# Kernel optimization log

Measured on AMD Instinct MI355X. Metric: run time of the kernel, lower is better.

## Reference

```python
import jax, jax.numpy as jnp
import numpy as np

DG = 8            # deformable_groups
MAX_RES = 10.0    # max_residual_magnitude
K = 9             # 3x3 kernel positions


def conv3(x, w, b):
    y = jax.lax.conv_general_dilated(x, w, (1, 1), [(1, 1), (1, 1)],
                                     dimension_numbers=('NCHW', 'OIHW', 'NCHW'))
    return y + b[None, :, None, None]


def lrelu(v):
    return jnp.where(v >= 0, v, 0.1 * v)


def deform_conv2d(x, offset, mask, weight, bias):
    # x: [B,C,H,W]; offset: [B,2*DG*K,H,W] (per group, K points, (y,x) interleaved)
    # mask: [B,DG*K,H,W]; weight: [O,C,3,3]; stride=1, pad=1, dil=1, groups=1
    B, C, H, W = x.shape
    Cg = C // DG
    off = offset.reshape(B, DG, K, 2, H, W)
    dtype = x.dtype
    dy = (jnp.arange(K) // 3 - 1).astype(dtype)
    dx = (jnp.arange(K) % 3 - 1).astype(dtype)
    py = off[:, :, :, 0] + jnp.arange(H, dtype=dtype)[None, None, None, :, None] + dy[None, None, :, None, None]
    px = off[:, :, :, 1] + jnp.arange(W, dtype=dtype)[None, None, None, None, :] + dx[None, None, :, None, None]
    y0 = jnp.floor(py)
    x0 = jnp.floor(px)
    x_flat = x.reshape(B, DG, Cg, H * W)
    m = mask.reshape(B, DG, K, H, W)
    acc = jnp.zeros((B, DG, Cg, K, H, W), dtype=dtype)
    for iy, wy in ((y0, y0 + 1.0 - py), (y0 + 1.0, py - y0)):
        for ix, wx in ((x0, x0 + 1.0 - px), (x0 + 1.0, px - x0)):
            valid = (iy >= 0) & (iy < H) & (ix >= 0) & (ix < W)
            yi = jnp.clip(iy, 0, H - 1).astype(jnp.int32)
            xi = jnp.clip(ix, 0, W - 1).astype(jnp.int32)
            idx = (yi * W + xi).reshape(B, DG, 1, K * H * W)
            g = jnp.take_along_axis(x_flat, idx, axis=3).reshape(B, DG, Cg, K, H, W)
            wgt = (wy * wx * valid.astype(dtype) * m)[:, :, None]  # mask folded in
            acc = acc + g * wgt
    O = weight.shape[0]
    out = jnp.einsum('bgckhw,ogck->bohw', acc, weight.reshape(O, DG, Cg, K))
    return out + bias[None, :, None, None]


def setup_inputs() -> dict:
    key = jax.random.key(0)
    ks = jax.random.split(key, 12)
    B, C, H, W = 4, 64, 128, 128
    inp = {
        'x': jax.random.normal(ks[0], (B, C, H, W), jnp.float32),
        'x_warped0': jax.random.normal(ks[1], (B, C, H, W), jnp.float32),
        'x_current': jax.random.normal(ks[2], (B, C, H, W), jnp.float32),
        'flow0': jax.random.normal(ks[3], (B, 2, H, W), jnp.float32),
        'w1': jax.random.normal(ks[4], (64, 130, 3, 3), jnp.float32) * 0.05,
        'b1': jnp.zeros((64,), jnp.float32),
        'w2': jax.random.normal(ks[5], (64, 64, 3, 3), jnp.float32) * 0.05,
        'b2': jnp.zeros((64,), jnp.float32),
        'w3': jax.random.normal(ks[6], (64, 64, 3, 3), jnp.float32) * 0.05,
        'b3': jnp.zeros((64,), jnp.float32),
        'w4': jax.random.normal(ks[7], (216, 64, 3, 3), jnp.float32) * 0.05,
        'b4': jnp.zeros((216,), jnp.float32),
        'weight': jax.random.normal(ks[8], (64, 64, 3, 3), jnp.float32) * 0.05,
        'bias': jnp.zeros((64,), jnp.float32),
    }
    return inp


def reference(x, x_warped0, x_current, flow0, w1, b1, w2, b2, w3, b3, w4, b4, weight, bias):
    # conv_offset stack on cat([x_warped0, x_current, flow0])
    feat = jnp.concatenate([x_warped0, x_current, flow0], axis=1)  # [B, 2C+2, H, W]
    o = lrelu(conv3(feat, w1, b1))
    o = lrelu(conv3(o, w2, b2))
    o = lrelu(conv3(o, w3, b3))
    o = conv3(o, w4, b4)  # [B, 3*K*DG, H, W]
    out1, out2, mask = jnp.split(o, 3, axis=1)
    offset = MAX_RES * jnp.tanh(jnp.concatenate([out1, out2], axis=1))  # [B, 2*K*DG, H, W]
    # flows[0].flip(1).repeat(1, K*DG, 1, 1): (y,x) flow tiled over all sample points
    offset = offset + jnp.tile(flow0[:, ::-1], (1, K * DG, 1, 1))
    mask = jax.nn.sigmoid(mask)
    return deform_conv2d(x, offset, mask, weight, bias)
```

## Files before the change

### kernel.cpp

```cpp
#include <hip/hip_runtime.h>
#include <math.h>

#define HH 128
#define WW 128
#define BB 4
#define HW (HH*WW)

typedef unsigned short u16;
typedef unsigned int u32;
typedef __bf16 bf16x8 __attribute__((ext_vector_type(8)));
typedef float f32x4 __attribute__((ext_vector_type(4)));

__device__ __forceinline__ u16 f2bf(float x) {
    u32 u = __float_as_uint(x);
    return (u16)((u + 0x7fffu + ((u >> 16) & 1u)) >> 16);
}
__device__ __forceinline__ float bf2f(u16 h) {
    return __uint_as_float(((u32)h) << 16);
}
__device__ __forceinline__ bf16x8 ld8(const u16* p) {
    union { uint4 u; bf16x8 v; } c;
    c.u = *(const uint4*)p;
    return c.v;
}
__device__ __forceinline__ bf16x8 cvt8(uint4 u) {
    union { uint4 u; bf16x8 v; } c;
    c.u = u;
    return c.v;
}

__global__ void split_w_k(const float* __restrict__ src, u16* __restrict__ dh,
                          u16* __restrict__ dl, int OC, int OCpad, int CIN, int CINpad)
{
    const int i = blockIdx.x * 256 + threadIdx.x;
    const int tot = OCpad * 9 * CINpad;
    if (i >= tot) return;
    const int oc = i / (9 * CINpad);
    const int r = i - oc * 9 * CINpad;
    const int tap = r / CINpad;
    const int cin = r - tap * CINpad;
    float v = 0.f;
    if (oc < OC && cin < CIN) v = src[((size_t)oc * CIN + cin) * 9 + tap];
    const u16 h = f2bf(v);
    dh[i] = h;
    dl[i] = f2bf(v - bf2f(h));
}

__global__ void pad_bias_k(const float* __restrict__ b, float* __restrict__ bp)
{
    const int i = blockIdx.x * 256 + threadIdx.x;
    if (i < 256) bp[i] = (i < 216) ? b[i] : 0.f;
}

__global__ void pack_dw_k(const float* __restrict__ wt, u16* __restrict__ Apack)
{
    const int i = blockIdx.x * 256 + threadIdx.x;
    if (i >= 36864) return;
    const int jj = i & 7;
    const int fr = (i >> 3) & 15;
    const int m  = (i >> 7) & 3;
    const int fq = (i >> 9) & 3;
    const int kk = i >> 11;
    const int oc = m * 16 + fr;
    const int j  = kk * 32 + fq * 8 + jj;
    const int tap = j >> 3, c = j & 7;
    const int g = tap / 9, kt = tap - g * 9;
    const int ch = g * 8 + c;
    Apack[i] = f2bf(wt[((size_t)oc * 64 + ch) * 9 + kt]);
}

template<int CREC>
__global__ __launch_bounds__(256) void pack_x_k(
    const float* __restrict__ A, const float* __restrict__ B2,
    const float* __restrict__ C3, u16* __restrict__ dst)
{
    const int i = blockIdx.x * 256 + threadIdx.x;
    const int b = i >> 14;
    const int px = i & 16383;
    u16* rec = dst + (size_t)i * (CREC * 2);

#pragma unroll
    for (int g = 0; g < CREC / 32; ++g) {
#pragma unroll
        for (int cb = 0; cb < 4; ++cb) {
            u32 hwv[4], lwv[4];
#pragma unroll
            for (int p = 0; p < 4; ++p) {
                float v[2];
#pragma unroll
                for (int e = 0; e < 2; ++e) {
                    const int c = g * 32 + cb * 8 + p * 2 + e;
                    float vv;
                    if (c < 64)       vv = A[((size_t)(b * 64 + c)) * HW + px];
                    else if (c < 128) vv = B2[((size_t)(b * 64 + c - 64)) * HW + px];
                    else if (c < 130) vv = C3[((size_t)(b * 2 + c - 128)) * HW + px];
                    else              vv = 0.f;
                    v[e] = vv;
                }
                const u16 h0 = f2bf(v[0]), h1 = f2bf(v[1]);
                const u16 l0 = f2bf(v[0] - bf2f(h0)), l1 = f2bf(v[1] - bf2f(h1));
                hwv[p] = (u32)h0 | ((u32)h1 << 16);
                lwv[p] = (u32)l0 | ((u32)l1 << 16);
            }
            uint4 H; H.x = hwv[0]; H.y = hwv[1]; H.z = hwv[2]; H.w = hwv[3];
            uint4 L; L.x = lwv[0]; L.y = lwv[1]; L.z = lwv[2]; L.w = lwv[3];
            *(uint4*)(rec + g * 64 + cb * 16)     = H;
            *(uint4*)(rec + g * 64 + cb * 16 + 8) = L;
        }
    }
}

template<int NCHUNK, int KGLAST, int MODE, bool RELU, bool PACKOUT, int MINW>
__global__ __launch_bounds__(256, MINW) void conv_pk_k(
    const u16* __restrict__ Xp, const u16* __restrict__ Wh, const u16* __restrict__ Wl,
    const float* __restrict__ bias, float* __restrict__ outf, u16* __restrict__ outp,
    int OCreal)
{
    const int ROWS = (MODE == 1) ? 8 : 4;
    const int NPX = (ROWS + 2) * 18;
    __shared__ u16 Xs[NPX * 136];
    const int CINpad = (NCHUNK - 1) * 64 + KGLAST * 32;
    const int CRECU16 = CINpad * 2;

    const int tile = blockIdx.x;
    const int h0 = (tile >> 3) * ROWS;
    const int w0 = (tile & 7) * 16;
    const int b = blockIdx.z;
    const int t = threadIdx.x;
    const int lane = t & 63, wv = t >> 6;
    const int fr = lane & 15, fq = lane >> 4;

    const int mg = wv >> 1, rg = wv & 1;
    const int mbase = (MODE == 1) ? (blockIdx.y * 8 + mg * 4) : 0;

    f32x4 acc0[4];
    f32x4 acc1[4][4];
    if (MODE == 0) {
        const float4 bv = *(const float4*)(bias + wv * 16 + 4 * fq);
#pragma unroll
        for (int n = 0; n < 4; ++n) {
            acc0[n][0] = bv.x; acc0[n][1] = bv.y; acc0[n][2] = bv.z; acc0[n][3] = bv.w;
        }
    } else {
#pragma unroll
        for (int m = 0; m < 4; ++m) {
            const float4 bv = *(const float4*)(bias + (mbase + m) * 16 + 4 * fq);
#pragma unroll
            for (int n = 0; n < 4; ++n) {
                acc1[m][n][0] = bv.x; acc1[m][n][1] = bv.y;
                acc1[m][n][2] = bv.z; acc1[m][n][3] = bv.w;
            }
        }
    }

    const u16* WhL = Wh + (size_t)fr * 9 * CINpad + 8 * fq;
    const u16* WlL = Wl + (size_t)fr * 9 * CINpad + 8 * fq;

#pragma unroll
    for (int chunk = 0; chunk < NCHUNK; ++chunk) {
        const int nkg = (chunk == NCHUNK - 1) ? KGLAST : 2;
        const int nu = nkg * 8;
        __syncthreads();
        for (int s = t; s < NPX * nu; s += 256) {
            const int px = s / nu, o = s - px * nu;
            const int hy = px / 18, hx = px - hy * 18;
            const int gy = h0 + hy - 1, gx = w0 + hx - 1;
            uint4 v; v.x = 0; v.y = 0; v.z = 0; v.w = 0;
            if (gy >= 0 && gy < HH && gx >= 0 && gx < WW)
                v = *(const uint4*)(Xp + ((size_t)(b * HW + gy * WW + gx)) * CRECU16
                                       + chunk * 128 + o * 8);
            *(uint4*)(Xs + px * 136 + o * 8) = v;
        }
        __syncthreads();

        if (MODE == 0) {
#pragma unroll
            for (int tap = 0; tap < 9; ++tap) {
                const int ky = tap / 3, kx = tap % 3;
#pragma unroll
                for (int kg = 0; kg < 2; ++kg) {
                    if (kg >= nkg) break;
                    const size_t off = (size_t)(wv * 144 + tap) * CINpad + chunk * 64 + kg * 32;
                    const bf16x8 Ah = ld8(WhL + off);
                    const bf16x8 Al = ld8(WlL + off);
#pragma unroll
                    for (int n = 0; n < 4; ++n) {
                        const int hp = (n + ky) * 18 + fr + kx;
                        const u16* Bp = Xs + hp * 136 + kg * 64 + fq * 16;
                        const bf16x8 Bh = ld8(Bp);
                        const bf16x8 Bl = ld8(Bp + 8);
                        acc0[n] = __builtin_amdgcn_mfma_f32_16x16x32_bf16(Ah, Bh, acc0[n], 0, 0, 0);
                        acc0[n] = __builtin_amdgcn_mfma_f32_16x16x32_bf16(Ah, Bl, acc0[n], 0, 0, 0);
                        acc0[n] = __builtin_amdgcn_mfma_f32_16x16x32_bf16(Al, Bh, acc0[n], 0, 0, 0);
                    }
                }
            }
        } else {
            auto PF = [&](int tap, bf16x8 (&Dh)[8], bf16x8 (&Dl)[8]) {
#pragma unroll
                for (int kg = 0; kg < 2; ++kg)
#pragma unroll
                    for (int m = 0; m < 4; ++m) {
                        const size_t off = (size_t)((mbase + m) * 144 + tap) * CINpad
                                         + chunk * 64 + kg * 32;
                        Dh[kg * 4 + m] = ld8(WhL + off);
                        Dl[kg * 4 + m] = ld8(WlL + off);
                    }
            };
            auto CMP = [&](int tap, bf16x8 (&Dh)[8], bf16x8 (&Dl)[8]) {
                const int ky = tap / 3, kx = tap - 3 * ky;
#pragma unroll
                for (int kg = 0; kg < 2; ++kg) {
#pragma unroll
                    for (int n = 0; n < 4; ++n) {
                        const int hp = (rg * 4 + n + ky) * 18 + fr + kx;
                        const u16* Bp = Xs + hp * 136 + kg * 64 + fq * 16;
                        const bf16x8 Bh = ld8(Bp);
                        const bf16x8 Bl = ld8(Bp + 8);
#pragma unroll
                        for (int m = 0; m < 4; ++m) {
                            acc1[m][n] = __builtin_amdgcn_mfma_f32_16x16x32_bf16(Dh[kg * 4 + m], Bh, acc1[m][n], 0, 0, 0);
                            acc1[m][n] = __builtin_amdgcn_mfma_f32_16x16x32_bf16(Dh[kg * 4 + m], Bl, acc1[m][n], 0, 0, 0);
                            acc1[m][n] = __builtin_amdgcn_mfma_f32_16x16x32_bf16(Dl[kg * 4 + m], Bh, acc1[m][n], 0, 0, 0);
                        }
                    }
                }
            };

            bf16x8 PaH[8], PaL[8], PbH[8], PbL[8];
            PF(0, PaH, PaL);
#pragma unroll 1
            for (int tp = 0; tp < 4; ++tp) {
                PF(2 * tp + 1, PbH, PbL);
                CMP(2 * tp, PaH, PaL);
                PF(2 * tp + 2, PaH, PaL);
                CMP(2 * tp + 1, PbH, PbL);
            }
            CMP(8, PaH, PaL);
        }
    }

    if (MODE == 1) {
#pragma unroll
        for (int m = 0; m < 4; ++m)
#pragma unroll
            for (int n = 0; n < 4; ++n)
#pragma unroll
                for (int i = 0; i < 4; ++i) {
                    const int oc = (mbase + m) * 16 + 4 * fq + i;
                    if (oc < OCreal) {
                        float v = acc1[m][n][i];
                        if (RELU) v = (v >= 0.f) ? v : 0.1f * v;
                        outf[((size_t)(b * OCreal + oc)) * HW + (h0 + rg * 4 + n) * WW + w0 + fr] = v;
                    }
                }
    } else if (!PACKOUT) {
#pragma unroll
        for (int n = 0; n < 4; ++n)
#pragma unroll
            for (int i = 0; i < 4; ++i) {
                const int oc = wv * 16 + 4 * fq + i;
                if (oc < OCreal) {
                    float v = acc0[n][i];
                    if (RELU) v = (v >= 0.f) ? v : 0.1f * v;
                    outf[((size_t)(b * OCreal + oc)) * HW + (h0 + n) * WW + w0 + fr] = v;
                }
            }
    } else {
        __syncthreads();
        const int coff = (wv >> 1) * 64 + (((wv << 1) + (fq >> 1)) & 3) * 16 + ((fq & 1) << 2);
#pragma unroll
        for (int n = 0; n < 4; ++n) {
            u16 hh[4], ll[4];
#pragma unroll
            for (int i = 0; i < 4; ++i) {
                float v = acc0[n][i];
                if (RELU) v = (v >= 0.f) ? v : 0.1f * v;
                hh[i] = f2bf(v);
                ll[i] = f2bf(v - bf2f(hh[i]));
            }
            uint2 H, L;
            H.x = (u32)hh[0] | ((u32)hh[1] << 16);
            H.y = (u32)hh[2] | ((u32)hh[3] << 16);
            L.x = (u32)ll[0] | ((u32)ll[1] << 16);
            L.y = (u32)ll[2] | ((u32)ll[3] << 16);
            const int pxe = n * 16 + fr;
            u16* E = Xs + pxe * 136 + coff;
            *(uint2*)E = H;
            *(uint2*)(E + 8) = L;
        }
        __syncthreads();
        for (int i = t; i < 1024; i += 256) {
            const int px = i >> 4, o = i & 15;
            const uint4 v = *(const uint4*)(Xs + px * 136 + o * 8);
            const int gp = (h0 + (px >> 4)) * WW + w0 + (px & 15);
            *(uint4*)(outp + ((size_t)(b * HW + gp)) * 128 + o * 8) = v;
        }
    }
}

__global__ __launch_bounds__(256) void pack_xb_k(
    const float* __restrict__ x, uint4* __restrict__ xqb)
{
    const int i = blockIdx.x * 256 + threadIdx.x;
    const int pix = i & (HW - 1);
    const int g = (i >> 14) & 7;
    const int b = i >> 17;
    const float* xp = x + ((size_t)(b * 64 + g * 8)) * HW + pix;
    u32 w[4];
#pragma unroll
    for (int c2 = 0; c2 < 4; ++c2) {
        const u16 l = f2bf(xp[(size_t)(2 * c2) * HW]);
        const u16 h = f2bf(xp[(size_t)(2 * c2 + 1) * HW]);
        w[c2] = (u32)l | ((u32)h << 16);
    }
    uint4 v; v.x = w[0]; v.y = w[1]; v.z = w[2]; v.w = w[3];
    xqb[(size_t)(b * 8 + g) * HW + pix] = v;
}

__device__ __forceinline__ unsigned pk_bf16(float lo, float hi) {
    unsigned a = __float_as_uint(lo), b = __float_as_uint(hi);
    return ((a + 0x8000u) >> 16) | ((b + 0x8000u) & 0xffff0000u);
}

__global__ __launch_bounds__(256, 4) void deform_fused_k(
    const uint4* __restrict__ xqb, const float* __restrict__ o4,
    const float* __restrict__ flow, const uint4* __restrict__ Apack,
    const float* __restrict__ bias, float* __restrict__ out)
{
    __shared__ u16 sv[32 * 584];

    const int bid = blockIdx.x;
    const int b = bid >> 9;
    const int pix0 = (bid & 511) << 5;
    const int t = threadIdx.x;

    {
        const int gpx = t & 31, g = t >> 5;
        const int pix = pix0 + gpx;
        const int h = pix >> 7, w = pix & (WW - 1);
        const float fy = flow[((size_t)b * 2 + 1) * HW + pix];
        const float fx = flow[((size_t)b * 2 + 0) * HW + pix];
        const float* ob = o4 + (size_t)b * 216 * HW + pix;
        const uint4* qg = xqb + (size_t)(b * 8 + g) * HW;

        int   code[9];
        float w00[9], w01[9], w10[9], w11[9];

#pragma unroll
        for (int k = 0; k < 9; ++k) {
            const float oy = ob[(size_t)(g * 18 + k * 2) * HW];
            const float ox = ob[(size_t)(g * 18 + k * 2 + 1) * HW];
            float mm = ob[(size_t)(144 + g * 9 + k) * HW];
            mm = __builtin_amdgcn_rcpf(1.f + __expf(-mm));

            const float ay = fabsf(oy), ax = fabsf(ox);
            const float ey = __expf(-2.f * ay), ex = __expf(-2.f * ax);
            float ty = (1.f - ey) * __builtin_amdgcn_rcpf(1.f + ey);
            float tx = (1.f - ex) * __builtin_amdgcn_rcpf(1.f + ex);
            ty = copysignf(ty, oy); tx = copysignf(tx, ox);

            const float ppy = 10.f * ty + fy + (float)(h + k / 3 - 1);
            const float ppx = 10.f * tx + fx + (float)(w + k % 3 - 1);

            const float y0f = floorf(ppy), x0f = floorf(ppx);
            const float ly = ppy - y0f, lx = ppx - x0f;
            const int iy0 = (int)y0f, ix0 = (int)x0f;
            const int iy1 = iy0 + 1,  ix1 = ix0 + 1;

            const float vy0 = (iy0 >= 0 && iy0 < HH) ? 1.f : 0.f;
            const float vy1 = (iy1 >= 0 && iy1 < HH) ? 1.f : 0.f;
            const float vx0 = (ix0 >= 0 && ix0 < WW) ? 1.f : 0.f;
            const float vx1 = (ix1 >= 0 && ix1 < WW) ? 1.f : 0.f;

            const int cy0 = min(max(iy0, 0), HH - 1);
            const int cy1 = min(max(iy1, 0), HH - 1);
            const int cx0 = min(max(ix0, 0), WW - 1);
            const int cx1 = min(max(ix1, 0), WW - 1);

            w00[k] = (1.f - ly) * (1.f - lx) * vy0 * vx0 * mm;
            w01[k] = (1.f - ly) * lx         * vy0 * vx1 * mm;
            w10[k] = ly         * (1.f - lx) * vy1 * vx0 * mm;
            w11[k] = ly         * lx         * vy1 * vx1 * mm;

            code[k] = (cy0 * WW + cx0) | ((cx1 - cx0) << 14) | ((cy1 - cy0) << 15);
        }

        u16* svp = sv + gpx * 584 + g * 72;
#pragma unroll
        for (int k = 0; k < 9; ++k) {
            const int i00 = code[k] & 16383;
            const int i01 = i00 + ((code[k] >> 14) & 1);
            const int i10 = i00 + (((code[k] >> 15) & 1) << 7);
            const int i11 = i10 + ((code[k] >> 14) & 1);

            const uint4 A4 = qg[i00];
            const uint4 B4 = qg[i01];
            const uint4 C4 = qg[i10];
            const uint4 D4 = qg[i11];
            const float W00 = w00[k], W01 = w01[k], W10 = w10[k], W11 = w11[k];

            uint4 P;
            u32 pw[4];
#pragma unroll
            for (int c2 = 0; c2 < 4; ++c2) {
                const u32 aw = (&A4.x)[c2], bw = (&B4.x)[c2];
                const u32 cw = (&C4.x)[c2], dw = (&D4.x)[c2];
                const float alo = __uint_as_float(aw << 16), ahi = __uint_as_float(aw & 0xffff0000u);
                const float blo = __uint_as_float(bw << 16), bhi = __uint_as_float(bw & 0xffff0000u);
                const float clo = __uint_as_float(cw << 16), chi = __uint_as_float(cw & 0xffff0000u);
                const float dlo = __uint_as_float(dw << 16), dhi = __uint_as_float(dw & 0xffff0000u);
                const float slo = W00 * alo + W01 * blo + W10 * clo + W11 * dlo;
                const float shi = W00 * ahi + W01 * bhi + W10 * chi + W11 * dhi;
                pw[c2] = pk_bf16(slo, shi);
            }
            P.x = pw[0]; P.y = pw[1]; P.z = pw[2]; P.w = pw[3];
            *(uint4*)(svp + (size_t)k * 8) = P;
        }
    }
    __syncthreads();

    {
        const int lane = t & 63, wv = t >> 6;
        const int fr = lane & 15, fq = lane >> 4;

        f32x4 acc[2];
#pragma unroll
        for (int n = 0; n < 2; ++n) { acc[n][0] = 0.f; acc[n][1] = 0.f; acc[n][2] = 0.f; acc[n][3] = 0.f; }

#pragma unroll
        for (int kk = 0; kk < 18; ++kk) {
            const bf16x8 A = cvt8(Apack[((kk * 4 + fq) * 4 + wv) * 16 + fr]);
#pragma unroll
            for (int n = 0; n < 2; ++n) {
                const bf16x8 Bf = ld8(sv + (size_t)(n * 16 + fr) * 584 + kk * 32 + fq * 8);
                acc[n] = __builtin_amdgcn_mfma_f32_16x16x32_bf16(A, Bf, acc[n], 0, 0, 0);
            }
        }

        const float4 bv = *(const float4*)(bias + wv * 16 + 4 * fq);
        const float bb[4] = { bv.x, bv.y, bv.z, bv.w };
#pragma unroll
        for (int n = 0; n < 2; ++n) {
            const int pix = pix0 + n * 16 + fr;
#pragma unroll
            for (int i = 0; i < 4; ++i) {
                const int oc = wv * 16 + 4 * fq + i;
                out[((size_t)b * 64 + oc) * HW + pix] = acc[n][i] + bb[i];
            }
        }
    }
}

extern "C" void kernel_launch(void* const* d_in, const int* in_sizes, int n_in,
                              void* d_out, int out_size, void* d_ws, size_t ws_size,
                              hipStream_t stream)
{
    const float* x     = (const float*)d_in[0];
    const float* xw    = (const float*)d_in[1];
    const float* xc    = (const float*)d_in[2];
    const float* flow  = (const float*)d_in[3];
    const float* w1    = (const float*)d_in[4];
    const float* b1    = (const float*)d_in[5];
    const float* w2    = (const float*)d_in[6];
    const float* b2    = (const float*)d_in[7];
    const float* w3    = (const float*)d_in[8];
    const float* b3    = (const float*)d_in[9];
    const float* w4    = (const float*)d_in[10];
    const float* b4    = (const float*)d_in[11];
    const float* wt    = (const float*)d_in[12];
    const float* bias  = (const float*)d_in[13];
    float* out = (float*)d_out;

    char* ws = (char*)d_ws;
    u16*   X1p  = (u16*)(ws);
    float* o4   = (float*)(ws);
    u16*   buf1 = (u16*)(ws + 56623104);
    u16*   buf2 = (u16*)(ws + 73400320);
    u16* Apack = (u16*)(ws + 90177536);
    u16* W1h = (u16*)(ws + 90251264);
    u16* W1l = (u16*)(ws + 90435584);
    u16* W2h = (u16*)(ws + 90619904);
    u16* W2l = (u16*)(ws + 90693632);
    u16* W3h = (u16*)(ws + 90767360);
    u16* W3l = (u16*)(ws + 90841088);
    u16* W4h = (u16*)(ws + 90914816);
    u16* W4l = (u16*)(ws + 91209728);
    float* b4p = (float*)(ws + 91504640);

    const dim3 blk(256);

    split_w_k<<<dim3((64 * 9 * 160 + 255) / 256), blk, 0, stream>>>(w1, W1h, W1l, 64, 64, 130, 160);
    split_w_k<<<dim3((64 * 9 * 64 + 255) / 256), blk, 0, stream>>>(w2, W2h, W2l, 64, 64, 64, 64);
    split_w_k<<<dim3((64 * 9 * 64 + 255) / 256), blk, 0, stream>>>(w3, W3h, W3l, 64, 64, 64, 64);
    split_w_k<<<dim3((256 * 9 * 64 + 255) / 256), blk, 0, stream>>>(w4, W4h, W4l, 216, 256, 64, 64);
    pad_bias_k<<<dim3(1), blk, 0, stream>>>(b4, b4p);
    pack_dw_k<<<dim3(144), blk, 0, stream>>>(wt, Apack);

    pack_x_k<160><<<dim3(BB * HW / 256), blk, 0, stream>>>(xw, xc, flow, X1p);
    conv_pk_k<3, 1, 0, true, true, 2><<<dim3(256, 1, BB), blk, 0, stream>>>(
        X1p, W1h, W1l, b1, nullptr, buf1, 64);
    conv_pk_k<1, 2, 0, true, true, 2><<<dim3(256, 1, BB), blk, 0, stream>>>(
        buf1, W2h, W2l, b2, nullptr, buf2, 64);
    conv_pk_k<1, 2, 0, true, true, 2><<<dim3(256, 1, BB), blk, 0, stream>>>(
        buf2, W3h, W3l, b3, nullptr, buf1, 64);
    pack_xb_k<<<dim3(BB * 8 * HW / 256), blk, 0, stream>>>(x, (uint4*)buf2);
    conv_pk_k<1, 2, 1, false, false, 1><<<dim3(128, 2, BB), blk, 0, stream>>>(
        buf1, W4h, W4l, b4p, o4, nullptr, 216);

    deform_fused_k<<<dim3(BB * HW / 32), blk, 0, stream>>>(
        (const uint4*)buf2, o4, flow, (const uint4*)Apack, bias, out);
}
```

Before: 276.5 us.

## Trim padded conv4 M-tiles and widen deform kernel to 512 threads

The final offset conv is split into two launches: one covering 8 M-tiles (NJ=4) and one covering 6 M-tiles (NJ=3). Together they cover 14 of the previous 16 padded 16-row tiles (224 rows against 216 real channels), so less padded-channel MFMA work is done. The deform kernel now uses 512 threads per block. The 9 kernel taps are split between two thread halves (4 and 5 taps), which halves per-thread gather work, and each wave computes a single MFMA output tile. Block indices are also remapped with a swizzle. The cost is an extra launch and possibly higher register or occupancy pressure.

```diff
diff --git a/kernel.cpp b/kernel.cpp
--- a/kernel.cpp
+++ b/kernel.cpp
@@ -110,11 +110,11 @@
     }
 }
 
-template<int NCHUNK, int KGLAST, int MODE, bool RELU, bool PACKOUT, int MINW>
+template<int NCHUNK, int KGLAST, int MODE, bool RELU, bool PACKOUT, int MINW, int NJ>
 __global__ __launch_bounds__(256, MINW) void conv_pk_k(
     const u16* __restrict__ Xp, const u16* __restrict__ Wh, const u16* __restrict__ Wl,
     const float* __restrict__ bias, float* __restrict__ outf, u16* __restrict__ outp,
-    int OCreal)
+    int OCreal, int mtile0)
 {
     const int ROWS = (MODE == 1) ? 8 : 4;
     const int NPX = (ROWS + 2) * 18;
@@ -131,10 +131,10 @@
     const int fr = lane & 15, fq = lane >> 4;
 
     const int mg = wv >> 1, rg = wv & 1;
-    const int mbase = (MODE == 1) ? (blockIdx.y * 8 + mg * 4) : 0;
+    const int mbase = (MODE == 1) ? (mtile0 + mg * NJ) : 0;
 
     f32x4 acc0[4];
-    f32x4 acc1[4][4];
+    f32x4 acc1[NJ][4];
     if (MODE == 0) {
         const float4 bv = *(const float4*)(bias + wv * 16 + 4 * fq);
 #pragma unroll
@@ -143,7 +143,7 @@
         }
     } else {
 #pragma unroll
-        for (int m = 0; m < 4; ++m) {
+        for (int m = 0; m < NJ; ++m) {
             const float4 bv = *(const float4*)(bias + (mbase + m) * 16 + 4 * fq);
 #pragma unroll
             for (int n = 0; n < 4; ++n) {
@@ -196,18 +196,18 @@
                 }
             }
         } else {
-            auto PF = [&](int tap, bf16x8 (&Dh)[8], bf16x8 (&Dl)[8]) {
+            auto PF = [&](int tap, bf16x8 (&Dh)[2 * NJ], bf16x8 (&Dl)[2 * NJ]) {
 #pragma unroll
                 for (int kg = 0; kg < 2; ++kg)
 #pragma unroll
-                    for (int m = 0; m < 4; ++m) {
+                    for (int m = 0; m < NJ; ++m) {
                         const size_t off = (size_t)((mbase + m) * 144 + tap) * CINpad
                                          + chunk * 64 + kg * 32;
-                        Dh[kg * 4 + m] = ld8(WhL + off);
-                        Dl[kg * 4 + m] = ld8(WlL + off);
+                        Dh[kg * NJ + m] = ld8(WhL + off);
+                        Dl[kg * NJ + m] = ld8(WlL + off);
                     }
             };
-            auto CMP = [&](int tap, bf16x8 (&Dh)[8], bf16x8 (&Dl)[8]) {
+            auto CMP = [&](int tap, bf16x8 (&Dh)[2 * NJ], bf16x8 (&Dl)[2 * NJ]) {
                 const int ky = tap / 3, kx = tap - 3 * ky;
 #pragma unroll
                 for (int kg = 0; kg < 2; ++kg) {
@@ -218,16 +218,16 @@
                         const bf16x8 Bh = ld8(Bp);
                         const bf16x8 Bl = ld8(Bp + 8);
 #pragma unroll
-                        for (int m = 0; m < 4; ++m) {
-                            acc1[m][n] = __builtin_amdgcn_mfma_f32_16x16x32_bf16(Dh[kg * 4 + m], Bh, acc1[m][n], 0, 0, 0);
-                            acc1[m][n] = __builtin_amdgcn_mfma_f32_16x16x32_bf16(Dh[kg * 4 + m], Bl, acc1[m][n], 0, 0, 0);
-                            acc1[m][n] = __builtin_amdgcn_mfma_f32_16x16x32_bf16(Dl[kg * 4 + m], Bh, acc1[m][n], 0, 0, 0);
+                        for (int m = 0; m < NJ; ++m) {
+                            acc1[m][n] = __builtin_amdgcn_mfma_f32_16x16x32_bf16(Dh[kg * NJ + m], Bh, acc1[m][n], 0, 0, 0);
+                            acc1[m][n] = __builtin_amdgcn_mfma_f32_16x16x32_bf16(Dh[kg * NJ + m], Bl, acc1[m][n], 0, 0, 0);
+                            acc1[m][n] = __builtin_amdgcn_mfma_f32_16x16x32_bf16(Dl[kg * NJ + m], Bh, acc1[m][n], 0, 0, 0);
                         }
                     }
                 }
             };
 
-            bf16x8 PaH[8], PaL[8], PbH[8], PbL[8];
+            bf16x8 PaH[2 * NJ], PaL[2 * NJ], PbH[2 * NJ], PbL[2 * NJ];
             PF(0, PaH, PaL);
 #pragma unroll 1
             for (int tp = 0; tp < 4; ++tp) {
@@ -242,7 +242,7 @@
 
     if (MODE == 1) {
 #pragma unroll
-        for (int m = 0; m < 4; ++m)
+        for (int m = 0; m < NJ; ++m)
 #pragma unroll
             for (int n = 0; n < 4; ++n)
 #pragma unroll
@@ -323,20 +323,24 @@
     return ((a + 0x8000u) >> 16) | ((b + 0x8000u) & 0xffff0000u);
 }
 
-__global__ __launch_bounds__(256, 4) void deform_fused_k(
+__global__ __launch_bounds__(512, 8) void deform_fused_k(
     const uint4* __restrict__ xqb, const float* __restrict__ o4,
     const float* __restrict__ flow, const uint4* __restrict__ Apack,
     const float* __restrict__ bias, float* __restrict__ out)
 {
     __shared__ u16 sv[32 * 584];
 
-    const int bid = blockIdx.x;
+    const int bid0 = blockIdx.x;
+    const int bid = (bid0 & 7) * 256 + (bid0 >> 3);
     const int b = bid >> 9;
     const int pix0 = (bid & 511) << 5;
     const int t = threadIdx.x;
 
     {
-        const int gpx = t & 31, g = t >> 5;
+        const int gpx = t & 31;
+        const int g = (t >> 5) & 7;
+        const int kh = t >> 8;
+        const int kbase = kh * 4;
         const int pix = pix0 + gpx;
         const int h = pix >> 7, w = pix & (WW - 1);
         const float fy = flow[((size_t)b * 2 + 1) * HW + pix];
@@ -344,11 +348,13 @@
         const float* ob = o4 + (size_t)b * 216 * HW + pix;
         const uint4* qg = xqb + (size_t)(b * 8 + g) * HW;
 
-        int   code[9];
-        float w00[9], w01[9], w10[9], w11[9];
-
-#pragma unroll
-        for (int k = 0; k < 9; ++k) {
+        int   code[5];
+        float w00[5], w01[5], w10[5], w11[5];
+
+#pragma unroll
+        for (int j = 0; j < 5; ++j) {
+            if (j == 4 && !kh) break;
+            const int k = kbase + j;
             const float oy = ob[(size_t)(g * 18 + k * 2) * HW];
             const float ox = ob[(size_t)(g * 18 + k * 2 + 1) * HW];
             float mm = ob[(size_t)(144 + g * 9 + k) * HW];
@@ -378,27 +384,28 @@
             const int cx0 = min(max(ix0, 0), WW - 1);
             const int cx1 = min(max(ix1, 0), WW - 1);
 
-            w00[k] = (1.f - ly) * (1.f - lx) * vy0 * vx0 * mm;
-            w01[k] = (1.f - ly) * lx         * vy0 * vx1 * mm;
-            w10[k] = ly         * (1.f - lx) * vy1 * vx0 * mm;
-            w11[k] = ly         * lx         * vy1 * vx1 * mm;
-
-            code[k] = (cy0 * WW + cx0) | ((cx1 - cx0) << 14) | ((cy1 - cy0) << 15);
-        }
-
-        u16* svp = sv + gpx * 584 + g * 72;
-#pragma unroll
-        for (int k = 0; k < 9; ++k) {
-            const int i00 = code[k] & 16383;
-            const int i01 = i00 + ((code[k] >> 14) & 1);
-            const int i10 = i00 + (((code[k] >> 15) & 1) << 7);
-            const int i11 = i10 + ((code[k] >> 14) & 1);
+            w00[j] = (1.f - ly) * (1.f - lx) * vy0 * vx0 * mm;
+            w01[j] = (1.f - ly) * lx         * vy0 * vx1 * mm;
+            w10[j] = ly         * (1.f - lx) * vy1 * vx0 * mm;
+            w11[j] = ly         * lx         * vy1 * vx1 * mm;
+
+            code[j] = (cy0 * WW + cx0) | ((cx1 - cx0) << 14) | ((cy1 - cy0) << 15);
+        }
+
+        u16* svp = sv + gpx * 584 + g * 72 + kbase * 8;
+#pragma unroll
+        for (int j = 0; j < 5; ++j) {
+            if (j == 4 && !kh) break;
+            const int i00 = code[j] & 16383;
+            const int i01 = i00 + ((code[j] >> 14) & 1);
+            const int i10 = i00 + (((code[j] >> 15) & 1) << 7);
+            const int i11 = i10 + ((code[j] >> 14) & 1);
 
             const uint4 A4 = qg[i00];
             const uint4 B4 = qg[i01];
             const uint4 C4 = qg[i10];
             const uint4 D4 = qg[i11];
-            const float W00 = w00[k], W01 = w01[k], W10 = w10[k], W11 = w11[k];
+            const float W00 = w00[j], W01 = w01[j], W10 = w10[j], W11 = w11[j];
 
             uint4 P;
             u32 pw[4];
@@ -415,39 +422,33 @@
                 pw[c2] = pk_bf16(slo, shi);
             }
             P.x = pw[0]; P.y = pw[1]; P.z = pw[2]; P.w = pw[3];
-            *(uint4*)(svp + (size_t)k * 8) = P;
+            *(uint4*)(svp + (size_t)j * 8) = P;
         }
     }
     __syncthreads();
 
     {
         const int lane = t & 63, wv = t >> 6;
+        const int mt = wv & 3, nt = wv >> 2;
         const int fr = lane & 15, fq = lane >> 4;
 
-        f32x4 acc[2];
-#pragma unroll
-        for (int n = 0; n < 2; ++n) { acc[n][0] = 0.f; acc[n][1] = 0.f; acc[n][2] = 0.f; acc[n][3] = 0.f; }
+        f32x4 acc;
+        acc[0] = 0.f; acc[1] = 0.f; acc[2] = 0.f; acc[3] = 0.f;
 
 #pragma unroll
         for (int kk = 0; kk < 18; ++kk) {
-            const bf16x8 A = cvt8(Apack[((kk * 4 + fq) * 4 + wv) * 16 + fr]);
-#pragma unroll
-            for (int n = 0; n < 2; ++n) {
-                const bf16x8 Bf = ld8(sv + (size_t)(n * 16 + fr) * 584 + kk * 32 + fq * 8);
-                acc[n] = __builtin_amdgcn_mfma_f32_16x16x32_bf16(A, Bf, acc[n], 0, 0, 0);
-            }
-        }
-
-        const float4 bv = *(const float4*)(bias + wv * 16 + 4 * fq);
+            const bf16x8 A = cvt8(Apack[((kk * 4 + fq) * 4 + mt) * 16 + fr]);
+            const bf16x8 Bf = ld8(sv + (size_t)(nt * 16 + fr) * 584 + kk * 32 + fq * 8);
+            acc = __builtin_amdgcn_mfma_f32_16x16x32_bf16(A, Bf, acc, 0, 0, 0);
+        }
+
+        const float4 bv = *(const float4*)(bias + mt * 16 + 4 * fq);
         const float bb[4] = { bv.x, bv.y, bv.z, bv.w };
-#pragma unroll
-        for (int n = 0; n < 2; ++n) {
-            const int pix = pix0 + n * 16 + fr;
-#pragma unroll
-            for (int i = 0; i < 4; ++i) {
-                const int oc = wv * 16 + 4 * fq + i;
-                out[((size_t)b * 64 + oc) * HW + pix] = acc[n][i] + bb[i];
-            }
+        const int pix = pix0 + nt * 16 + fr;
+#pragma unroll
+        for (int i = 0; i < 4; ++i) {
+            const int oc = mt * 16 + 4 * fq + i;
+            out[((size_t)b * 64 + oc) * HW + pix] = acc[i] + bb[i];
         }
     }
 }
@@ -498,16 +499,18 @@
     pack_dw_k<<<dim3(144), blk, 0, stream>>>(wt, Apack);
 
     pack_x_k<160><<<dim3(BB * HW / 256), blk, 0, stream>>>(xw, xc, flow, X1p);
-    conv_pk_k<3, 1, 0, true, true, 2><<<dim3(256, 1, BB), blk, 0, stream>>>(
-        X1p, W1h, W1l, b1, nullptr, buf1, 64);
-    conv_pk_k<1, 2, 0, true, true, 2><<<dim3(256, 1, BB), blk, 0, stream>>>(
-        buf1, W2h, W2l, b2, nullptr, buf2, 64);
-    conv_pk_k<1, 2, 0, true, true, 2><<<dim3(256, 1, BB), blk, 0, stream>>>(
-        buf2, W3h, W3l, b3, nullptr, buf1, 64);
+    conv_pk_k<3, 1, 0, true, true, 2, 4><<<dim3(256, 1, BB), blk, 0, stream>>>(
+        X1p, W1h, W1l, b1, nullptr, buf1, 64, 0);
+    conv_pk_k<1, 2, 0, true, true, 2, 4><<<dim3(256, 1, BB), blk, 0, stream>>>(
+        buf1, W2h, W2l, b2, nullptr, buf2, 64, 0);
+    conv_pk_k<1, 2, 0, true, true, 2, 4><<<dim3(256, 1, BB), blk, 0, stream>>>(
+        buf2, W3h, W3l, b3, nullptr, buf1, 64, 0);
     pack_xb_k<<<dim3(BB * 8 * HW / 256), blk, 0, stream>>>(x, (uint4*)buf2);
-    conv_pk_k<1, 2, 1, false, false, 1><<<dim3(128, 2, BB), blk, 0, stream>>>(
-        buf1, W4h, W4l, b4p, o4, nullptr, 216);
-
-    deform_fused_k<<<dim3(BB * HW / 32), blk, 0, stream>>>(
+    conv_pk_k<1, 2, 1, false, false, 1, 4><<<dim3(128, 1, BB), blk, 0, stream>>>(
+        buf1, W4h, W4l, b4p, o4, nullptr, 216, 0);
+    conv_pk_k<1, 2, 1, false, false, 1, 3><<<dim3(128, 1, BB), blk, 0, stream>>>(
+        buf1, W4h, W4l, b4p, o4, nullptr, 216, 8);
+
+    deform_fused_k<<<dim3(BB * HW / 32), dim3(512), 0, stream>>>(
         (const uint4*)buf2, o4, flow, (const uint4*)Apack, bias, out);
 }
```

Result: no change. 280.1 us (+1.3%).
